# Optimization experiments

Measured on AMD Instinct MI355X. Metric: run time of the kernel, lower is better.

## Reference

```python
import jax, jax.numpy as jnp
import numpy as np

NEG = -1e9  # sentinel for suppressed / below-threshold scores
SCORE_THRESHOLD = 0.05
IOU_THRESHOLD = 0.5
MAX_DETECTIONS = 100


def _iou_one_vs_all(box, boxes):
    # box: (4,) in (x1, y1, x2, y2); boxes: (N, 4)
    ix1 = jnp.maximum(box[0], boxes[:, 0])
    iy1 = jnp.maximum(box[1], boxes[:, 1])
    ix2 = jnp.minimum(box[2], boxes[:, 2])
    iy2 = jnp.minimum(box[3], boxes[:, 3])
    inter = jnp.maximum(ix2 - ix1, 0.0) * jnp.maximum(iy2 - iy1, 0.0)
    a1 = (box[2] - box[0]) * (box[3] - box[1])
    a2 = (boxes[:, 2] - boxes[:, 0]) * (boxes[:, 3] - boxes[:, 1])
    return inter / jnp.maximum(a1 + a2 - inter, 1e-8)


def _nms_single_class(boxes, scores):
    # boxes: (N, 4), scores: (N,). Fixed-shape greedy NMS via scan.
    scores0 = jnp.where(scores > SCORE_THRESHOLD, scores, NEG)

    def step(s, _):
        best = jnp.argmax(s)
        bscore = s[best]
        bbox = boxes[best]
        iou = _iou_one_vs_all(bbox, boxes)
        # suppress overlapping boxes (incl. the selected one, IoU=1)
        s_next = jnp.where(iou > IOU_THRESHOLD, NEG, s)
        return s_next, (bscore, bbox)

    _, (keep_scores, keep_boxes) = jax.lax.scan(step, scores0, None, length=MAX_DETECTIONS)
    return keep_scores, keep_boxes  # (M,), (M, 4)


def _filter_one_image(boxes, classification):
    # boxes: (N, 4), classification: (N, C)
    C = classification.shape[1]
    cls_scores = classification.T  # (C, N)
    ks, kb = jax.vmap(lambda s: _nms_single_class(boxes, s))(cls_scores)  # (C, M), (C, M, 4)
    labels = jnp.broadcast_to(jnp.arange(C, dtype=jnp.int32)[:, None], ks.shape)
    scores_flat = ks.reshape(-1)          # (C*M,)
    boxes_flat = kb.reshape(-1, 4)        # (C*M, 4)
    labels_flat = labels.reshape(-1)      # (C*M,)
    top_scores, top_idx = jax.lax.top_k(scores_flat, MAX_DETECTIONS)
    top_boxes = boxes_flat[top_idx]
    top_labels = labels_flat[top_idx]
    valid = top_scores > SCORE_THRESHOLD
    out_scores = jnp.where(valid, top_scores, -1.0)
    out_boxes = jnp.where(valid[:, None], top_boxes, -1.0)
    out_labels = jnp.where(valid, top_labels, -1).astype(jnp.int32)
    return out_boxes, out_scores, out_labels


def setup_inputs() -> dict:
    key = jax.random.key(0)
    k1, k2, k3 = jax.random.split(key, 3)
    B, N, C = 2, 10000, 80
    xy = jax.random.uniform(k1, (B, N, 2), dtype=jnp.float32) * 900.0
    wh = jax.random.uniform(k2, (B, N, 2), dtype=jnp.float32) * 100.0 + 1.0
    boxes = jnp.concatenate([xy, xy + wh], axis=-1)  # valid (x1,y1,x2,y2)
    # raise to 4th power so most scores fall below the 0.05 threshold (realistic)
    classification = jax.random.uniform(k3, (B, N, C), dtype=jnp.float32) ** 4
    return {"boxes": boxes, "classification": classification}


@jax.jit
def reference(boxes, classification):
    # boxes: (B, N, 4), classification: (B, N, C)
    out_boxes, out_scores, out_labels = jax.vmap(_filter_one_image)(boxes, classification)
    return out_boxes, out_scores, out_labels
```

## Files before the change

kernel.cpp:

```cpp
#include <hip/hip_runtime.h>
#include <hip/hip_bf16.h>
#include <float.h>
#include <stdint.h>

#pragma clang fp contract(off)

#define NEGV   (-1e9f)
#define THRV   (0.05f)
#define MAXDET 100
#define NB     1152
#define BKBASE 31385
#define SLAB   7168
#define TKCAP  1024

__device__ __forceinline__ int bktOf(unsigned u) {
  int v = (int)(u >> 15) - BKBASE;
  return v < 0 ? 0 : (v > NB - 1 ? NB - 1 : v);
}

__device__ __forceinline__ bool killpair(
    float qx1, float qy1, float qx2, float qy2, float qa,
    float x1, float y1, float x2, float y2, float a)
{
  const float iw = fminf(qx2, x2) - fmaxf(qx1, x1);
  const float ih = fminf(qy2, y2) - fmaxf(qy1, y1);
  if (iw <= 0.f || ih <= 0.f) return false;
  const float inter = iw * ih;
  const float den = fmaxf((qa + a) - inter, 1e-8f);
  const float i2 = inter + inter;
  if (i2 > den * 1.00001f) return true;
  if (i2 < den * 0.99999f) return false;
  return (inter / den) > 0.5f;
}

template<int BT>
__device__ __forceinline__ int suffix_scan(int* hist, int* wtot,
                                           int tid, int lane, int wid) {
  int c0 = 0, c1 = 0, c2 = 0;
  if (tid < NB / 3) {
    c0 = hist[NB - 1 - 3 * tid];
    c1 = hist[NB - 2 - 3 * tid];
    c2 = hist[NB - 3 - 3 * tid];
  }
  const int tsum = c0 + c1 + c2;
  int inc = tsum;
#pragma unroll
  for (int off = 1; off < 64; off <<= 1) {
    const int u = __shfl_up(inc, off, 64);
    if (lane >= off) inc += u;
  }
  if (lane == 63) wtot[wid] = inc;
  __syncthreads();
  int wbase = 0, tot = 0;
#pragma unroll
  for (int w = 0; w < BT / 64; ++w) {
    const int v = wtot[w];
    if (w < wid) wbase += v;
    tot += v;
  }
  const int excl = wbase + inc - tsum;
  if (tid < NB / 3) {
    hist[NB - 1 - 3 * tid] = excl;
    hist[NB - 2 - 3 * tid] = excl + c0;
    hist[NB - 3 - 3 * tid] = excl + c0 + c1;
  }
  __syncthreads();
  return tot;
}

__global__ __launch_bounds__(256, 1) void transpose_kernel(
    const float* __restrict__ cls, float* __restrict__ clsT, int N, int C)
{
  __shared__ float tile[32][33];
  const int b = blockIdx.z;
  const int n0 = blockIdx.x * 32, c0 = blockIdx.y * 32;
  const int tx = threadIdx.x, ty = threadIdx.y;
#pragma unroll
  for (int r = ty; r < 32; r += 8) {
    const int n = n0 + r, c = c0 + tx;
    if (n < N && c < C) tile[r][tx] = cls[((size_t)b * N + n) * C + c];
  }
  __syncthreads();
#pragma unroll
  for (int r = ty; r < 32; r += 8) {
    const int c = c0 + r, n = n0 + tx;
    if (n < N && c < C) clsT[((size_t)b * C + c) * N + n] = tile[tx][r];
  }
}

template<int BT>
__global__ __launch_bounds__(BT, 1) void nms_kernel(
    const float* __restrict__ boxes, const float* __restrict__ clsT,
    unsigned long long* __restrict__ skg_all,
    float* __restrict__ ksc, float* __restrict__ kbx, int N, int C)
{
#pragma clang fp contract(off)
  const int bc = blockIdx.x;
  const int tid = threadIdx.x, lane = tid & 63, wid = tid >> 6;

  const float* ct = clsT + (size_t)bc * N;
  const float4* bb4 = (const float4*)(boxes + (size_t)(bc / C) * N * 4);
  unsigned long long* skg = skg_all + (size_t)bc * N;

  __shared__ unsigned long long slab[SLAB];
  __shared__ int hist[NB];
  __shared__ int wtot[BT / 64];
  __shared__ float4 kboxS[MAXDET];
  __shared__ float  kscoreS[MAXDET];
  __shared__ float  kareaS[MAXDET];
  __shared__ unsigned long long wkill[BT / 64];
  __shared__ unsigned long long killby[64];

  for (int i = tid; i < NB; i += BT) hist[i] = 0;
  __syncthreads();
  for (int i = tid; i < N; i += BT) {
    const float s = ct[i];
    if (s > THRV) atomicAdd(&hist[bktOf(__float_as_uint(s))], 1);
  }
  __syncthreads();

  const int cn = suffix_scan<BT>(hist, wtot, tid, lane, wid);

  for (int i = tid; i < N; i += BT) {
    const float s = ct[i];
    if (s > THRV) {
      const unsigned u = __float_as_uint(s);
      const int pos = atomicAdd(&hist[bktOf(u)], 1);
      const unsigned long long key =
          ((unsigned long long)u << 32) | (unsigned)(~i);
      if (pos < SLAB) slab[pos] = key; else skg[pos] = key;
    }
  }
  __syncthreads();

  for (int bk = tid; bk < NB; bk += BT) {
    const int lo = (bk == NB - 1) ? 0 : hist[bk + 1];
    const int hi = hist[bk];
    for (int x = lo + 1; x < hi; ++x) {
      const unsigned long long v = (x < SLAB) ? slab[x] : skg[x];
      int y = x - 1;
      while (y >= lo) {
        const unsigned long long w = (y < SLAB) ? slab[y] : skg[y];
        if (w >= v) break;
        if (y + 1 < SLAB) slab[y + 1] = w; else skg[y + 1] = w;
        --y;
      }
      if (y + 1 < SLAB) slab[y + 1] = v; else skg[y + 1] = v;
    }
  }
  __syncthreads();

  int nk = 0;
  for (int base = 0; base < cn && nk < MAXDET; base += 64) {
    const int nc = min(64, cn - base);
    const bool valid = lane < nc;
    const int p = base + lane;
    unsigned long long key = 0ull;
    if (valid) key = (p < SLAB) ? slab[p] : skg[p];
    const float score = __uint_as_float((unsigned)(key >> 32));
    const int idx = (int)(~(unsigned)key);
    float4 bx = make_float4(0.f, 0.f, 0.f, 0.f);
    if (valid) bx = bb4[idx];
    const float area = (bx.z - bx.x) * (bx.w - bx.y);

    bool kill = false;
    for (int e = wid; e < nk; e += BT / 64) {
      const float4 q = kboxS[e];
      kill = kill || killpair(q.x, q.y, q.z, q.w, kareaS[e],
                              bx.x, bx.y, bx.z, bx.w, area);
    }
    {
      const unsigned long long bm = __ballot(valid && kill);
      if (lane == 0) wkill[wid] = bm;
    }
    {
      const int cb = wid * 8;
#pragma unroll
      for (int jj = 0; jj < 8; ++jj) {
        const int j = cb + jj;
        if (j < nc) {
          const float jx1 = __int_as_float(__builtin_amdgcn_readlane(__float_as_int(bx.x), j));
          const float jy1 = __int_as_float(__builtin_amdgcn_readlane(__float_as_int(bx.y), j));
          const float jx2 = __int_as_float(__builtin_amdgcn_readlane(__float_as_int(bx.z), j));
          const float jy2 = __int_as_float(__builtin_amdgcn_readlane(__float_as_int(bx.w), j));
          const float ja  = __int_as_float(__builtin_amdgcn_readlane(__float_as_int(area), j));
          const bool kij = valid && killpair(jx1, jy1, jx2, jy2, ja,
                                             bx.x, bx.y, bx.z, bx.w, area);
          const unsigned long long bm = __ballot(kij);
          if (lane == 0) killby[j] = bm;
        }
      }
    }
    __syncthreads();

    unsigned long long kmask = 0;
#pragma unroll
    for (int w = 0; w < BT / 64; ++w) kmask |= wkill[w];
    unsigned long long alive = ~kmask;
    alive &= (nc >= 64) ? ~0ull : ((1ull << nc) - 1ull);
    const unsigned long long kb = killby[lane];
    for (int j = 0; j < 64; ++j) {
      if ((alive >> j) & 1ull) {
        const unsigned klo = (unsigned)__builtin_amdgcn_readlane((int)(unsigned)kb, j);
        const unsigned khi = (unsigned)__builtin_amdgcn_readlane((int)(unsigned)(kb >> 32), j);
        const unsigned long long km = ((unsigned long long)khi << 32) | klo;
        alive &= ~(km & ((~1ull) << j));
      }
    }
    if (wid == 0) {
      const int rank = (int)__popcll(alive & ((1ull << lane) - 1ull));
      if (((alive >> lane) & 1ull) && (nk + rank < MAXDET)) {
        kboxS[nk + rank] = bx;
        kscoreS[nk + rank] = score;
        kareaS[nk + rank] = area;
      }
    }
    nk += min((int)__popcll(alive), MAXDET - nk);
    __syncthreads();
  }

  float* ko  = ksc + (size_t)bc * MAXDET;
  float* kbo = kbx + (size_t)bc * MAXDET * 4;
  for (int e = tid; e < MAXDET; e += BT) {
    if (e < nk) {
      const float4 q = kboxS[e];
      ko[e] = kscoreS[e];
      kbo[e * 4 + 0] = q.x; kbo[e * 4 + 1] = q.y;
      kbo[e * 4 + 2] = q.z; kbo[e * 4 + 3] = q.w;
    } else {
      ko[e] = NEGV;
      kbo[e * 4 + 0] = 0.f; kbo[e * 4 + 1] = 0.f;
      kbo[e * 4 + 2] = 0.f; kbo[e * 4 + 3] = 0.f;
    }
  }
}

template<int BT>
__global__ __launch_bounds__(BT, 1) void topk_kernel(
    const float* __restrict__ ksc, const float* __restrict__ kbx,
    unsigned long long* __restrict__ gcand_all,
    float* __restrict__ out, int B, int C)
{
  const int b = blockIdx.x;
  const int tid = threadIdx.x, lane = tid & 63, wid = tid >> 6;
  const int T = C * MAXDET;
  const float* s0 = ksc + (size_t)b * T;
  unsigned long long* gc = gcand_all + (size_t)b * T;
  float* ob = out;
  float* os = out + (size_t)B * MAXDET * 4;
  float* ol = os + (size_t)B * MAXDET;

  __shared__ int hist[NB];
  __shared__ int wtot[BT / 64];
  __shared__ unsigned long long cand[TKCAP];
  __shared__ int tB, cposS;

  for (int i = tid; i < NB; i += BT) hist[i] = 0;
  if (tid == 0) { cposS = 0; tB = 0; }
  __syncthreads();
  for (int f = tid; f < T; f += BT) {
    const float s = s0[f];
    if (s > THRV) atomicAdd(&hist[bktOf(__float_as_uint(s))], 1);
  }
  __syncthreads();
  suffix_scan<BT>(hist, wtot, tid, lane, wid);
  for (int bk = tid; bk < NB; bk += BT)
    if (hist[bk] < MAXDET && (bk == 0 || hist[bk - 1] >= MAXDET)) tB = bk;
  __syncthreads();
  const int t = tB;
  for (int f = tid; f < T; f += BT) {
    const float s = s0[f];
    if (s > THRV) {
      const unsigned u = __float_as_uint(s);
      if (bktOf(u) >= t) {
        const int p = atomicAdd(&cposS, 1);
        const unsigned long long key =
            ((unsigned long long)u << 32) | (unsigned)(~f);
        if (p < TKCAP) cand[p] = key; else gc[p] = key;
      }
    }
  }
  __syncthreads();
  const int nc = cposS;
  const int nw = min(nc, MAXDET);
  for (int s2 = nw + tid; s2 < MAXDET; s2 += BT) {
    float* od = ob + ((size_t)b * MAXDET + s2) * 4;
    od[0] = -1.f; od[1] = -1.f; od[2] = -1.f; od[3] = -1.f;
    os[(size_t)b * MAXDET + s2] = -1.f;
    ol[(size_t)b * MAXDET + s2] = -1.f;
  }
  for (int e = tid; e < nc; e += BT) {
    const unsigned long long k = (e < TKCAP) ? cand[e] : gc[e];
    int rank = 0;
    for (int j = 0; j < nc; ++j) {
      const unsigned long long o = (j < TKCAP) ? cand[j] : gc[j];
      rank += (o > k) ? 1 : 0;
    }
    if (rank < MAXDET) {
      const int f = (int)(~(unsigned)k);
      const float sc = __uint_as_float((unsigned)(k >> 32));
      const float* bp = kbx + ((size_t)b * T + f) * 4;
      float* od = ob + ((size_t)b * MAXDET + rank) * 4;
      od[0] = bp[0]; od[1] = bp[1]; od[2] = bp[2]; od[3] = bp[3];
      os[(size_t)b * MAXDET + rank] = sc;
      ol[(size_t)b * MAXDET + rank] = (float)(f / MAXDET);
    }
  }
}

extern "C" void kernel_launch(void* const* d_in, const int* in_sizes, int n_in,
                              void* d_out, int out_size, void* d_ws, size_t ws_size,
                              hipStream_t stream) {
  const float* boxes = (const float*)d_in[0];
  const float* cls   = (const float*)d_in[1];
  const int B = out_size / (MAXDET * 6);
  const int N = in_sizes[0] / (B * 4);
  const int C = in_sizes[1] / (B * N);

  char* ws = (char*)d_ws;
  float* clsT = (float*)ws; ws += (size_t)B * C * N * 4;
  float* kbx = (float*)ws;  ws += (size_t)B * C * MAXDET * 16;
  float* ksc = (float*)ws;  ws += (size_t)B * C * MAXDET * 4;
  unsigned long long* gcand = (unsigned long long*)ws;
  ws += (size_t)B * C * MAXDET * 8;
  unsigned long long* skg = (unsigned long long*)ws;

  transpose_kernel<<<dim3((N + 31) / 32, (C + 31) / 32, B), dim3(32, 8),
                     0, stream>>>(cls, clsT, N, C);
  nms_kernel<512><<<dim3(B * C), dim3(512), 0, stream>>>(
      boxes, clsT, skg, ksc, kbx, N, C);
  topk_kernel<512><<<dim3(B), dim3(512), 0, stream>>>(
      ksc, kbx, gcand, (float*)d_out, B, C);
}
```

Measured before the change: 154.4 us.

## Sort only top score chunk per class with rank sort, fall back to full path

The NMS kernel now finds the highest score buckets holding at least a target count of candidates, scatters only those into shared memory, and rank-sorts them before the greedy scan. A full histogram, scatter and insertion sort in global memory runs only when that chunk is too large or does not yield enough detections. NMS also writes a per-image histogram of kept scores so the top-k kernel can skip its own histogram pass. Block size rises to 1024 threads. The cost is an extra memset launch, global atomics per kept box, and an O(n^2) rank sort over the chunk.

Result: slower. 159.6 us (+3.4%).

```diff
diff --git a/kernel.cpp b/kernel.cpp
--- a/kernel.cpp
+++ b/kernel.cpp
@@ -1,5 +1,4 @@
 #include <hip/hip_runtime.h>
-#include <hip/hip_bf16.h>
 #include <float.h>
 #include <stdint.h>
 
@@ -10,7 +9,8 @@
 #define MAXDET 100
 #define NB     1152
 #define BKBASE 31385
-#define SLAB   7168
+#define SLABSZ 1024
+#define CHTGT  512
 #define TKCAP  1024
 
 __device__ __forceinline__ int bktOf(unsigned u) {
@@ -68,95 +68,24 @@
   return tot;
 }
 
-__global__ __launch_bounds__(256, 1) void transpose_kernel(
-    const float* __restrict__ cls, float* __restrict__ clsT, int N, int C)
-{
-  __shared__ float tile[32][33];
-  const int b = blockIdx.z;
-  const int n0 = blockIdx.x * 32, c0 = blockIdx.y * 32;
-  const int tx = threadIdx.x, ty = threadIdx.y;
-#pragma unroll
-  for (int r = ty; r < 32; r += 8) {
-    const int n = n0 + r, c = c0 + tx;
-    if (n < N && c < C) tile[r][tx] = cls[((size_t)b * N + n) * C + c];
-  }
-  __syncthreads();
-#pragma unroll
-  for (int r = ty; r < 32; r += 8) {
-    const int c = c0 + r, n = n0 + tx;
-    if (n < N && c < C) clsT[((size_t)b * C + c) * N + n] = tile[tx][r];
-  }
-}
-
 template<int BT>
-__global__ __launch_bounds__(BT, 1) void nms_kernel(
-    const float* __restrict__ boxes, const float* __restrict__ clsT,
-    unsigned long long* __restrict__ skg_all,
-    float* __restrict__ ksc, float* __restrict__ kbx, int N, int C)
+__device__ int run_scan(
+    const unsigned long long* kL, const unsigned long long* kG, bool useL,
+    int cn, const float4* __restrict__ bb4,
+    float4* kboxS, float* kscoreS, float* kareaS,
+    unsigned long long* wkill, unsigned long long* killby,
+    int tid, int lane, int wid)
 {
 #pragma clang fp contract(off)
-  const int bc = blockIdx.x;
-  const int tid = threadIdx.x, lane = tid & 63, wid = tid >> 6;
-
-  const float* ct = clsT + (size_t)bc * N;
-  const float4* bb4 = (const float4*)(boxes + (size_t)(bc / C) * N * 4);
-  unsigned long long* skg = skg_all + (size_t)bc * N;
-
-  __shared__ unsigned long long slab[SLAB];
-  __shared__ int hist[NB];
-  __shared__ int wtot[BT / 64];
-  __shared__ float4 kboxS[MAXDET];
-  __shared__ float  kscoreS[MAXDET];
-  __shared__ float  kareaS[MAXDET];
-  __shared__ unsigned long long wkill[BT / 64];
-  __shared__ unsigned long long killby[64];
-
-  for (int i = tid; i < NB; i += BT) hist[i] = 0;
-  __syncthreads();
-  for (int i = tid; i < N; i += BT) {
-    const float s = ct[i];
-    if (s > THRV) atomicAdd(&hist[bktOf(__float_as_uint(s))], 1);
-  }
-  __syncthreads();
-
-  const int cn = suffix_scan<BT>(hist, wtot, tid, lane, wid);
-
-  for (int i = tid; i < N; i += BT) {
-    const float s = ct[i];
-    if (s > THRV) {
-      const unsigned u = __float_as_uint(s);
-      const int pos = atomicAdd(&hist[bktOf(u)], 1);
-      const unsigned long long key =
-          ((unsigned long long)u << 32) | (unsigned)(~i);
-      if (pos < SLAB) slab[pos] = key; else skg[pos] = key;
-    }
-  }
-  __syncthreads();
-
-  for (int bk = tid; bk < NB; bk += BT) {
-    const int lo = (bk == NB - 1) ? 0 : hist[bk + 1];
-    const int hi = hist[bk];
-    for (int x = lo + 1; x < hi; ++x) {
-      const unsigned long long v = (x < SLAB) ? slab[x] : skg[x];
-      int y = x - 1;
-      while (y >= lo) {
-        const unsigned long long w = (y < SLAB) ? slab[y] : skg[y];
-        if (w >= v) break;
-        if (y + 1 < SLAB) slab[y + 1] = w; else skg[y + 1] = w;
-        --y;
-      }
-      if (y + 1 < SLAB) slab[y + 1] = v; else skg[y + 1] = v;
-    }
-  }
-  __syncthreads();
-
+  constexpr int NW = BT / 64;
+  constexpr int CPW = 64 / NW;
   int nk = 0;
   for (int base = 0; base < cn && nk < MAXDET; base += 64) {
     const int nc = min(64, cn - base);
     const bool valid = lane < nc;
     const int p = base + lane;
     unsigned long long key = 0ull;
-    if (valid) key = (p < SLAB) ? slab[p] : skg[p];
+    if (valid) key = useL ? kL[p] : kG[p];
     const float score = __uint_as_float((unsigned)(key >> 32));
     const int idx = (int)(~(unsigned)key);
     float4 bx = make_float4(0.f, 0.f, 0.f, 0.f);
@@ -164,7 +93,7 @@
     const float area = (bx.z - bx.x) * (bx.w - bx.y);
 
     bool kill = false;
-    for (int e = wid; e < nk; e += BT / 64) {
+    for (int e = wid; e < nk; e += NW) {
       const float4 q = kboxS[e];
       kill = kill || killpair(q.x, q.y, q.z, q.w, kareaS[e],
                               bx.x, bx.y, bx.z, bx.w, area);
@@ -174,9 +103,9 @@
       if (lane == 0) wkill[wid] = bm;
     }
     {
-      const int cb = wid * 8;
-#pragma unroll
-      for (int jj = 0; jj < 8; ++jj) {
+      const int cb = wid * CPW;
+#pragma unroll
+      for (int jj = 0; jj < CPW; ++jj) {
         const int j = cb + jj;
         if (j < nc) {
           const float jx1 = __int_as_float(__builtin_amdgcn_readlane(__float_as_int(bx.x), j));
@@ -195,7 +124,7 @@
 
     unsigned long long kmask = 0;
 #pragma unroll
-    for (int w = 0; w < BT / 64; ++w) kmask |= wkill[w];
+    for (int w = 0; w < NW; ++w) kmask |= wkill[w];
     unsigned long long alive = ~kmask;
     alive &= (nc >= 64) ? ~0ull : ((1ull << nc) - 1ull);
     const unsigned long long kb = killby[lane];
@@ -218,15 +147,144 @@
     nk += min((int)__popcll(alive), MAXDET - nk);
     __syncthreads();
   }
+  return nk;
+}
+
+__global__ __launch_bounds__(256, 1) void transpose_kernel(
+    const float* __restrict__ cls, float* __restrict__ clsT, int N, int C)
+{
+  __shared__ float tile[32][33];
+  const int b = blockIdx.z;
+  const int n0 = blockIdx.x * 32, c0 = blockIdx.y * 32;
+  const int tx = threadIdx.x, ty = threadIdx.y;
+#pragma unroll
+  for (int r = ty; r < 32; r += 8) {
+    const int n = n0 + r, c = c0 + tx;
+    if (n < N && c < C) tile[r][tx] = cls[((size_t)b * N + n) * C + c];
+  }
+  __syncthreads();
+#pragma unroll
+  for (int r = ty; r < 32; r += 8) {
+    const int c = c0 + r, n = n0 + tx;
+    if (n < N && c < C) clsT[((size_t)b * C + c) * N + n] = tile[tx][r];
+  }
+}
+
+template<int BT>
+__global__ __launch_bounds__(BT, 1) void nms_kernel(
+    const float* __restrict__ boxes, const float* __restrict__ clsT,
+    unsigned long long* __restrict__ skg_all,
+    float* __restrict__ ksc, float* __restrict__ kbx,
+    int* __restrict__ ihist, int N, int C)
+{
+#pragma clang fp contract(off)
+  const int bc = blockIdx.x;
+  const int tid = threadIdx.x, lane = tid & 63, wid = tid >> 6;
+
+  const float* ct = clsT + (size_t)bc * N;
+  const float4* bb4 = (const float4*)(boxes + (size_t)(bc / C) * N * 4);
+  unsigned long long* skg = skg_all + (size_t)bc * N;
+
+  __shared__ unsigned long long slab[SLABSZ];
+  __shared__ unsigned long long sorted[SLABSZ];
+  __shared__ int hist[NB];
+  __shared__ int wtot[BT / 64];
+  __shared__ float4 kboxS[MAXDET];
+  __shared__ float  kscoreS[MAXDET];
+  __shared__ float  kareaS[MAXDET];
+  __shared__ unsigned long long wkill[BT / 64];
+  __shared__ unsigned long long killby[64];
+  __shared__ int bkLoS;
+
+  for (int i = tid; i < NB; i += BT) hist[i] = 0;
+  if (tid == 0) bkLoS = -1;
+  __syncthreads();
+  for (int i = tid; i < N; i += BT) {
+    const float s = ct[i];
+    if (s > THRV) atomicAdd(&hist[bktOf(__float_as_uint(s))], 1);
+  }
+  __syncthreads();
+
+  const int cn = suffix_scan<BT>(hist, wtot, tid, lane, wid);
+
+  for (int bk = tid; bk < NB; bk += BT)
+    if (hist[bk] >= CHTGT) atomicMax(&bkLoS, bk);
+  __syncthreads();
+  const int bkLo = bkLoS;
+  const int chunkCnt = (bkLo >= 0) ? hist[bkLo] : cn;
+
+  int nk = 0;
+  bool slow = (chunkCnt > SLABSZ);
+  if (!slow) {
+    for (int i = tid; i < N; i += BT) {
+      const float s = ct[i];
+      if (s > THRV) {
+        const unsigned u = __float_as_uint(s);
+        const int bk = bktOf(u);
+        if (bk > bkLo) {
+          const int pos = atomicAdd(&hist[bk], 1);
+          slab[pos] = ((unsigned long long)u << 32) | (unsigned)(~i);
+        }
+      }
+    }
+    __syncthreads();
+    for (int e = tid; e < chunkCnt; e += BT) {
+      const unsigned long long k = slab[e];
+      int r = 0;
+      for (int j = 0; j < chunkCnt; ++j) r += (slab[j] > k) ? 1 : 0;
+      sorted[r] = k;
+    }
+    __syncthreads();
+    nk = run_scan<BT>(sorted, skg, true, chunkCnt, bb4,
+                      kboxS, kscoreS, kareaS, wkill, killby, tid, lane, wid);
+    slow = (nk < MAXDET && chunkCnt < cn);
+  }
+
+  if (slow) {
+    __syncthreads();
+    for (int i = tid; i < NB; i += BT) hist[i] = 0;
+    __syncthreads();
+    for (int i = tid; i < N; i += BT) {
+      const float s = ct[i];
+      if (s > THRV) atomicAdd(&hist[bktOf(__float_as_uint(s))], 1);
+    }
+    __syncthreads();
+    suffix_scan<BT>(hist, wtot, tid, lane, wid);
+    for (int i = tid; i < N; i += BT) {
+      const float s = ct[i];
+      if (s > THRV) {
+        const unsigned u = __float_as_uint(s);
+        const int pos = atomicAdd(&hist[bktOf(u)], 1);
+        skg[pos] = ((unsigned long long)u << 32) | (unsigned)(~i);
+      }
+    }
+    __syncthreads();
+    for (int bk = tid; bk < NB; bk += BT) {
+      const int lo = (bk == NB - 1) ? 0 : hist[bk + 1];
+      const int hi = hist[bk];
+      for (int x = lo + 1; x < hi; ++x) {
+        const unsigned long long v = skg[x];
+        int y = x - 1;
+        while (y >= lo && skg[y] < v) { skg[y + 1] = skg[y]; --y; }
+        skg[y + 1] = v;
+      }
+    }
+    __syncthreads();
+    nk = run_scan<BT>(sorted, skg, false, cn, bb4,
+                      kboxS, kscoreS, kareaS, wkill, killby, tid, lane, wid);
+  }
 
   float* ko  = ksc + (size_t)bc * MAXDET;
   float* kbo = kbx + (size_t)bc * MAXDET * 4;
+  int* ih = ihist + (size_t)(bc / C) * NB;
   for (int e = tid; e < MAXDET; e += BT) {
     if (e < nk) {
       const float4 q = kboxS[e];
-      ko[e] = kscoreS[e];
+      const float s = kscoreS[e];
+      ko[e] = s;
       kbo[e * 4 + 0] = q.x; kbo[e * 4 + 1] = q.y;
       kbo[e * 4 + 2] = q.z; kbo[e * 4 + 3] = q.w;
+      atomicAdd(&ih[bktOf(__float_as_uint(s))], 1);
     } else {
       ko[e] = NEGV;
       kbo[e * 4 + 0] = 0.f; kbo[e * 4 + 1] = 0.f;
@@ -238,7 +296,7 @@
 template<int BT>
 __global__ __launch_bounds__(BT, 1) void topk_kernel(
     const float* __restrict__ ksc, const float* __restrict__ kbx,
-    unsigned long long* __restrict__ gcand_all,
+    const int* __restrict__ ihist, unsigned long long* __restrict__ gcand_all,
     float* __restrict__ out, int B, int C)
 {
   const int b = blockIdx.x;
@@ -253,21 +311,16 @@
   __shared__ int hist[NB];
   __shared__ int wtot[BT / 64];
   __shared__ unsigned long long cand[TKCAP];
-  __shared__ int tB, cposS;
-
-  for (int i = tid; i < NB; i += BT) hist[i] = 0;
-  if (tid == 0) { cposS = 0; tB = 0; }
-  __syncthreads();
-  for (int f = tid; f < T; f += BT) {
-    const float s = s0[f];
-    if (s > THRV) atomicAdd(&hist[bktOf(__float_as_uint(s))], 1);
-  }
+  __shared__ int tBs, cposS;
+
+  for (int i = tid; i < NB; i += BT) hist[i] = ihist[(size_t)b * NB + i];
+  if (tid == 0) { cposS = 0; tBs = 0; }
   __syncthreads();
   suffix_scan<BT>(hist, wtot, tid, lane, wid);
   for (int bk = tid; bk < NB; bk += BT)
-    if (hist[bk] < MAXDET && (bk == 0 || hist[bk - 1] >= MAXDET)) tB = bk;
-  __syncthreads();
-  const int t = tB;
+    if (hist[bk] < MAXDET && (bk == 0 || hist[bk - 1] >= MAXDET)) tBs = bk;
+  __syncthreads();
+  const int t = tBs;
   for (int f = tid; f < T; f += BT) {
     const float s = s0[f];
     if (s > THRV) {
@@ -318,17 +371,20 @@
   const int C = in_sizes[1] / (B * N);
 
   char* ws = (char*)d_ws;
+  unsigned long long* skg = (unsigned long long*)ws;
+  ws += (size_t)B * C * N * 8;
+  unsigned long long* gcand = (unsigned long long*)ws;
+  ws += (size_t)B * C * MAXDET * 8;
   float* clsT = (float*)ws; ws += (size_t)B * C * N * 4;
   float* kbx = (float*)ws;  ws += (size_t)B * C * MAXDET * 16;
   float* ksc = (float*)ws;  ws += (size_t)B * C * MAXDET * 4;
-  unsigned long long* gcand = (unsigned long long*)ws;
-  ws += (size_t)B * C * MAXDET * 8;
-  unsigned long long* skg = (unsigned long long*)ws;
-
+  int* ihist = (int*)ws;
+
+  hipMemsetAsync(ihist, 0, (size_t)B * NB * 4, stream);
   transpose_kernel<<<dim3((N + 31) / 32, (C + 31) / 32, B), dim3(32, 8),
                      0, stream>>>(cls, clsT, N, C);
-  nms_kernel<512><<<dim3(B * C), dim3(512), 0, stream>>>(
-      boxes, clsT, skg, ksc, kbx, N, C);
-  topk_kernel<512><<<dim3(B), dim3(512), 0, stream>>>(
-      ksc, kbx, gcand, (float*)d_out, B, C);
-}
+  nms_kernel<1024><<<dim3(B * C), dim3(1024), 0, stream>>>(
+      boxes, clsT, skg, ksc, kbx, ihist, N, C);
+  topk_kernel<1024><<<dim3(B), dim3(1024), 0, stream>>>(
+      ksc, kbx, ihist, gcand, (float*)d_out, B, C);
+}
```
